# Optimization experiments

Hardware: AMD Instinct MI355X
Metric: run time of the kernel (lower is better)

The kernel has to match this reference:

```python
import jax, jax.numpy as jnp
import numpy as np

EPS_FEAT = 1e-4   # stabilizer eps inside favorp_projection
EPS_DEN = 0.01    # clamp_min eps for the attention denominator


def favorp_projection(data, projection_matrix, is_query):
    # data: [b, h, n, d]; projection_matrix: [h, m, d]
    d = data.shape[-1]
    data_normalizer = d ** (-0.25)
    ratio = projection_matrix.shape[1] ** (-0.5)
    data_dash = jnp.einsum('bhnd,hmd->bhnm', data_normalizer * data, projection_matrix)
    diag_data = (jnp.sum(data * data, axis=-1) * 0.5 * data_normalizer * data_normalizer)[..., None]
    if is_query:
        stabilizer = jax.lax.stop_gradient(jnp.max(data_dash, axis=-1, keepdims=True))
    else:
        stabilizer = jax.lax.stop_gradient(jnp.max(data_dash, axis=(-1, -2), keepdims=True))
    return ratio * jnp.exp(data_dash - diag_data - stabilizer) + EPS_FEAT


def setup_inputs() -> dict:
    key = jax.random.key(0)
    ks = jax.random.split(key, 12)
    N, B, E, H, D, M = 4096, 4, 1024, 16, 64, 64
    s = E ** -0.5
    return {
        'query': jax.random.normal(ks[0], (N, B, E), jnp.float32),
        'key': jax.random.normal(ks[1], (N, B, E), jnp.float32),
        'value': jax.random.normal(ks[2], (N, B, E), jnp.float32),
        'Wq': jax.random.normal(ks[3], (E, E), jnp.float32) * s,
        'bq': jax.random.normal(ks[4], (E,), jnp.float32) * 0.02,
        'Wk': jax.random.normal(ks[5], (E, E), jnp.float32) * s,
        'bk': jax.random.normal(ks[6], (E,), jnp.float32) * 0.02,
        'Wv': jax.random.normal(ks[7], (E, E), jnp.float32) * s,
        'bv': jax.random.normal(ks[8], (E,), jnp.float32) * 0.02,
        'Wo': jax.random.normal(ks[9], (E, E), jnp.float32) * s,
        'bo': jax.random.normal(ks[10], (E,), jnp.float32) * 0.02,
        'proj': jax.random.normal(ks[11], (H, M, D), jnp.float32),
    }


def reference(query, key, value, Wq, bq, Wk, bk, Wv, bv, Wo, bo, proj):
    H = proj.shape[0]
    # [n, b, e] -> [b, n, e]
    q_in = query.transpose(1, 0, 2)
    k_in = key.transpose(1, 0, 2)
    v_in = value.transpose(1, 0, 2)
    B, N, E = q_in.shape
    D = E // H

    def lin(x, W, b):
        return jnp.einsum('bne,fe->bnf', x, W) + b

    def split_heads(x):  # [b, n, e] -> [b, h, n, d]
        return x.reshape(B, N, H, D).transpose(0, 2, 1, 3)

    q = split_heads(lin(q_in, Wq, bq))
    k = split_heads(lin(k_in, Wk, bk))
    v = split_heads(lin(v_in, Wv, bv))

    q_prime = favorp_projection(q, proj, is_query=True)   # [b, h, n, m]
    k_prime = favorp_projection(k, proj, is_query=False)  # [b, h, n, m]

    # non-causal linear attention: O(n * m * d)
    kv = jnp.einsum('bhnm,bhnd->bhmd', k_prime, v)
    qkv = jnp.einsum('bhnm,bhmd->bhnd', q_prime, kv)
    normalizer = jnp.einsum('bhnm,bhm->bhn', q_prime, k_prime.sum(axis=2))
    output = qkv / jnp.maximum(normalizer[..., None], EPS_DEN)

    attn_output = output.transpose(0, 2, 1, 3).reshape(B, N, E)  # b h n d -> b n (h d)
    out = lin(attn_output, Wo, bo)
    return out.transpose(1, 0, 2)  # back to [n, b, e]
```

## Files before the change

kernel.cpp:

```cpp
#include <hip/hip_runtime.h>
#include <math.h>

#define B_   4
#define N_   4096
#define E_   1024
#define H_   16
#define BN_  (B_*N_)
#define BH_  (B_*H_)
#define SPLITK 8

#define NRM_C   0.35355339059327373f
#define DIAG_C  0.0625f
#define RATIO_C 0.125f
#define EPSF    1e-4f
#define EPSD    0.01f

typedef __attribute__((ext_vector_type(8))) short bf16x8;
typedef __attribute__((ext_vector_type(4))) float f32x4;

__device__ __forceinline__ unsigned short f32_to_bf16(float x) {
    unsigned int u = __float_as_uint(x);
    unsigned int r = (u + 0x7fffu + ((u >> 16) & 1u)) >> 16;
    return (unsigned short)r;
}
__device__ __forceinline__ float bf16_to_f32(unsigned short h) {
    return __uint_as_float(((unsigned int)h) << 16);
}

__device__ __forceinline__ void atomicMaxF(float* addr, float v) {
    if (v >= 0.f) atomicMax((int*)addr, __float_as_int(v));
    else          atomicMin((unsigned int*)addr, __float_as_uint(v));
}

__global__ void init_stab(float* stab) {
    if (threadIdx.x < BH_) stab[threadIdx.x] = -INFINITY;
}

template<int IN_MODE>
__global__ __launch_bounds__(256) void convert_split(const float* __restrict__ src,
                                                     unsigned short* __restrict__ hi,
                                                     unsigned short* __restrict__ lo,
                                                     int total4)
{
    int i = blockIdx.x * 256 + threadIdx.x;
    const int stride = gridDim.x * 256;
    for (; i < total4; i += stride) {
        long e4 = (long)i * 4;
        const float* p;
        if (IN_MODE == 0) {
            long r = e4 >> 10; int e = (int)(e4 & 1023);
            int b = (int)(r >> 12), n = (int)(r & 4095);
            p = src + (((long)(n * B_ + b)) << 10) + e;
        } else {
            p = src + e4;
        }
        float4 v = *(const float4*)p;
        ushort4 h, l;
        h.x = f32_to_bf16(v.x); l.x = f32_to_bf16(v.x - bf16_to_f32(h.x));
        h.y = f32_to_bf16(v.y); l.y = f32_to_bf16(v.y - bf16_to_f32(h.y));
        h.z = f32_to_bf16(v.z); l.z = f32_to_bf16(v.z - bf16_to_f32(h.z));
        h.w = f32_to_bf16(v.w); l.w = f32_to_bf16(v.w - bf16_to_f32(h.w));
        *(ushort4*)(hi + e4) = h;
        *(ushort4*)(lo + e4) = l;
    }
}

__device__ __forceinline__ void gl_lds16(const unsigned short* g, unsigned short* l) {
    __builtin_amdgcn_global_load_lds((const __attribute__((address_space(1))) void*)g,
                                     (__attribute__((address_space(3))) void*)l, 16, 0, 0);
}

#define SMEM_BYTES (4*64*68*4 + 2*4*64*4)

template<int MODE>
__global__ __launch_bounds__(256) void gemm_mfma(const unsigned short* __restrict__ Ahi,
                                                 const unsigned short* __restrict__ Alo,
                                                 const unsigned short* __restrict__ Bhi,
                                                 const unsigned short* __restrict__ Blo,
                                                 const float* __restrict__ bias,
                                                 float* __restrict__ Y,
                                                 float* __restrict__ stab,
                                                 const unsigned short* __restrict__ PShi,
                                                 const unsigned short* __restrict__ PSlo,
                                                 const unsigned short* __restrict__ kvThi,
                                                 const unsigned short* __restrict__ kvTlo,
                                                 const float* __restrict__ ksum,
                                                 unsigned short* __restrict__ AttnHi,
                                                 unsigned short* __restrict__ AttnLo)
{
    __shared__ __align__(16) char SMEM[SMEM_BYTES];
    unsigned short* smem = (unsigned short*)SMEM;
    const int t = threadIdx.x;
    const int w = t >> 6, lane = t & 63;
    const int row0 = blockIdx.x * 128, col0 = blockIdx.y * 128;
    const int wrow = (w >> 1) * 64, wcol = (w & 1) * 64;
    const int g = lane >> 4, rl = lane & 15;

    const int sr = w * 32 + (lane >> 2);
    const int kswz = (((lane & 3) ^ ((lane >> 2) & 3)) << 3);
    const long aoff = (long)(row0 + sr) * E_ + kswz;
    const long boff = (long)(col0 + sr) * E_ + kswz;

    f32x4 acc[4][4];
#pragma unroll
    for (int m = 0; m < 4; ++m)
#pragma unroll
        for (int n = 0; n < 4; ++n) acc[m][n] = (f32x4){0.f, 0.f, 0.f, 0.f};

#define STAGE_STEP(KS, BUF)                                                          \
    {                                                                                \
        const int k0 = (KS) * 32;                                                    \
        unsigned short* d = smem + (BUF) * 16384 + w * 1024;                         \
        gl_lds16(Ahi + aoff + k0,             d);                                    \
        gl_lds16(Ahi + aoff + k0 + 16 * E_,   d + 512);                              \
        gl_lds16(Alo + aoff + k0,             d + 4096);                             \
        gl_lds16(Alo + aoff + k0 + 16 * E_,   d + 4096 + 512);                       \
        gl_lds16(Bhi + boff + k0,             d + 8192);                             \
        gl_lds16(Bhi + boff + k0 + 16 * E_,   d + 8192 + 512);                       \
        gl_lds16(Blo + boff + k0,             d + 12288);                            \
        gl_lds16(Blo + boff + k0 + 16 * E_,   d + 12288 + 512);                      \
    }

    STAGE_STEP(0, 0);

    for (int ks = 0; ks < 32; ++ks) {
        __syncthreads();
        if (ks + 1 < 32) STAGE_STEP(ks + 1, (ks + 1) & 1);
        const unsigned short* sb = smem + (ks & 1) * 16384;
        bf16x8 ah[4], al[4], bh[4], bl[4];
#pragma unroll
        for (int m = 0; m < 4; ++m) {
            int r = wrow + m * 16 + rl;
            int off = r * 32 + ((g ^ (r & 3)) << 3);
            ah[m] = *(const bf16x8*)(sb + off);
            al[m] = *(const bf16x8*)(sb + 4096 + off);
        }
#pragma unroll
        for (int n = 0; n < 4; ++n) {
            int r = wcol + n * 16 + rl;
            int off = r * 32 + ((g ^ (r & 3)) << 3);
            bh[n] = *(const bf16x8*)(sb + 8192 + off);
            bl[n] = *(const bf16x8*)(sb + 12288 + off);
        }
#pragma unroll
        for (int m = 0; m < 4; ++m)
#pragma unroll
            for (int n = 0; n < 4; ++n)
                acc[m][n] = __builtin_amdgcn_mfma_f32_16x16x32_bf16(ah[m], bh[n], acc[m][n], 0, 0, 0);
#pragma unroll
        for (int m = 0; m < 4; ++m)
#pragma unroll
            for (int n = 0; n < 4; ++n)
                acc[m][n] = __builtin_amdgcn_mfma_f32_16x16x32_bf16(ah[m], bl[n], acc[m][n], 0, 0, 0);
#pragma unroll
        for (int m = 0; m < 4; ++m)
#pragma unroll
            for (int n = 0; n < 4; ++n)
                acc[m][n] = __builtin_amdgcn_mfma_f32_16x16x32_bf16(al[m], bh[n], acc[m][n], 0, 0, 0);
    }
#undef STAGE_STEP

    float bv[4];
#pragma unroll
    for (int n = 0; n < 4; ++n) bv[n] = bias[col0 + wcol + n * 16 + rl];

    if (MODE <= 1) {
#pragma unroll
        for (int m = 0; m < 4; ++m) {
            int rbase = row0 + wrow + m * 16 + g * 4;
#pragma unroll
            for (int n = 0; n < 4; ++n) {
                int c = col0 + wcol + n * 16 + rl;
#pragma unroll
                for (int q = 0; q < 4; ++q) {
                    int r = rbase + q;
                    float v = acc[m][n][q] + bv[n];
                    long off;
                    if (MODE == 0) off = (long)r * E_ + c;
                    else { int b = r >> 12, nn = r & (N_ - 1); off = (long)(nn * B_ + b) * E_ + c; }
                    Y[off] = v;
                }
            }
        }
        return;
    }

    __syncthreads();
    float* accF  = (float*)SMEM + w * (64 * 68);
    float* diagL = (float*)(SMEM + 4*64*68*4) + w * 64;
    float* rnmL  = (float*)(SMEM + 4*64*68*4) + 256 + w * 64;
    const int b_idx = row0 >> 12;
    const int hg = (col0 >> 6) + (w & 1);
    const int bh = b_idx * H_ + hg;

#pragma unroll
    for (int m = 0; m < 4; ++m)
#pragma unroll
        for (int n = 0; n < 4; ++n)
#pragma unroll
            for (int q = 0; q < 4; ++q)
                accF[(m*16 + g*4 + q) * 68 + n*16 + rl] = acc[m][n][q] + bv[n];
    {
        float s = 0.f;
#pragma unroll 16
        for (int d = 0; d < 64; ++d) { float x = accF[lane * 68 + d]; s = fmaf(x, x, s); }
        diagL[lane] = s * DIAG_C;
    }
    __syncthreads();

    float wavemax = -INFINITY;
#pragma unroll
    for (int mi = 0; mi < 4; ++mi) {
        bf16x8 dah[2], dal[2];
#pragma unroll
        for (int kk = 0; kk < 2; ++kk) {
            const float* src = &accF[(mi*16 + rl) * 68 + kk*32 + g*8];
            float4 f0 = *(const float4*)src, f1 = *(const float4*)(src + 4);
            float fv[8] = {f0.x,f0.y,f0.z,f0.w,f1.x,f1.y,f1.z,f1.w};
            bf16x8 hh, ll;
#pragma unroll
            for (int j = 0; j < 8; ++j) {
                unsigned short h16 = f32_to_bf16(fv[j]);
                hh[j] = (short)h16;
                ll[j] = (short)f32_to_bf16(fv[j] - bf16_to_f32(h16));
            }
            dah[kk] = hh; dal[kk] = ll;
        }
        f32x4 dacc[4];
#pragma unroll
        for (int n = 0; n < 4; ++n) dacc[n] = (f32x4){0.f,0.f,0.f,0.f};
#pragma unroll
        for (int n = 0; n < 4; ++n)
#pragma unroll
            for (int kk = 0; kk < 2; ++kk) {
                long po = (long)hg * 4096 + (n*16 + rl) * 64 + kk*32 + g*8;
                bf16x8 pbh = *(const bf16x8*)(PShi + po);
                bf16x8 pbl = *(const bf16x8*)(PSlo + po);
                dacc[n] = __builtin_amdgcn_mfma_f32_16x16x32_bf16(dah[kk], pbh, dacc[n], 0, 0, 0);
                dacc[n] = __builtin_amdgcn_mfma_f32_16x16x32_bf16(dah[kk], pbl, dacc[n], 0, 0, 0);
                dacc[n] = __builtin_amdgcn_mfma_f32_16x16x32_bf16(dal[kk], pbh, dacc[n], 0, 0, 0);
            }
        if (MODE == 2) {
#pragma unroll
            for (int n = 0; n < 4; ++n)
#pragma unroll
                for (int q = 0; q < 4; ++q) {
                    float dsh = dacc[n][q] * NRM_C;
                    wavemax = fmaxf(wavemax, dsh);
                    int rloc = mi*16 + g*4 + q;
                    Y[(long)(row0 + wrow + rloc) * E_ + col0 + wcol + n*16 + rl] = dsh - diagL[rloc];
                }
        } else {
            float rm0 = -INFINITY, rm1 = -INFINITY, rm2 = -INFINITY, rm3 = -INFINITY;
#pragma unroll
            for (int n = 0; n < 4; ++n) {
                rm0 = fmaxf(rm0, dacc[n][0]); rm1 = fmaxf(rm1, dacc[n][1]);
                rm2 = fmaxf(rm2, dacc[n][2]); rm3 = fmaxf(rm3, dacc[n][3]);
            }
#pragma unroll
            for (int off = 1; off < 16; off <<= 1) {
                rm0 = fmaxf(rm0, __shfl_xor(rm0, off));
                rm1 = fmaxf(rm1, __shfl_xor(rm1, off));
                rm2 = fmaxf(rm2, __shfl_xor(rm2, off));
                rm3 = fmaxf(rm3, __shfl_xor(rm3, off));
            }
            float rmq[4] = {rm0 * NRM_C, rm1 * NRM_C, rm2 * NRM_C, rm3 * NRM_C};
#pragma unroll
            for (int n = 0; n < 4; ++n)
#pragma unroll
                for (int q = 0; q < 4; ++q) {
                    int rloc = mi*16 + g*4 + q;
                    float qp = RATIO_C * expf(dacc[n][q] * NRM_C - diagL[rloc] - rmq[q]) + EPSF;
                    accF[rloc * 68 + n*16 + rl] = qp;
                }
        }
    }

    if (MODE == 2) {
#pragma unroll
        for (int off = 1; off < 64; off <<= 1) wavemax = fmaxf(wavemax, __shfl_xor(wavemax, off));
        if (lane == 0) atomicMaxF(&stab[bh], wavemax);
        return;
    }

    {
        float s = 0.f;
        const float* kb = ksum + bh * 64;
#pragma unroll 16
        for (int m = 0; m < 64; ++m) s = fmaf(accF[lane * 68 + m], kb[m], s);
        rnmL[lane] = 1.f / fmaxf(s, EPSD);
    }
    __syncthreads();
#pragma unroll
    for (int mi = 0; mi < 4; ++mi) {
        bf16x8 qah[2], qal[2];
#pragma unroll
        for (int kk = 0; kk < 2; ++kk) {
            const float* src = &accF[(mi*16 + rl) * 68 + kk*32 + g*8];
            float4 f0 = *(const float4*)src, f1 = *(const float4*)(src + 4);
            float fv[8] = {f0.x,f0.y,f0.z,f0.w,f1.x,f1.y,f1.z,f1.w};
            bf16x8 hh, ll;
#pragma unroll
            for (int j = 0; j < 8; ++j) {
                unsigned short h16 = f32_to_bf16(fv[j]);
                hh[j] = (short)h16;
                ll[j] = (short)f32_to_bf16(fv[j] - bf16_to_f32(h16));
            }
            qah[kk] = hh; qal[kk] = ll;
        }
        f32x4 oacc[4];
#pragma unroll
        for (int n = 0; n < 4; ++n) oacc[n] = (f32x4){0.f,0.f,0.f,0.f};
#pragma unroll
        for (int n = 0; n < 4; ++n)
#pragma unroll
            for (int kk = 0; kk < 2; ++kk) {
                long ko = (long)bh * 4096 + (n*16 + rl) * 64 + kk*32 + g*8;
                bf16x8 kbh = *(const bf16x8*)(kvThi + ko);
                bf16x8 kbl = *(const bf16x8*)(kvTlo + ko);
                oacc[n] = __builtin_amdgcn_mfma_f32_16x16x32_bf16(qah[kk], kbh, oacc[n], 0, 0, 0);
                oacc[n] = __builtin_amdgcn_mfma_f32_16x16x32_bf16(qah[kk], kbl, oacc[n], 0, 0, 0);
                oacc[n] = __builtin_amdgcn_mfma_f32_16x16x32_bf16(qal[kk], kbh, oacc[n], 0, 0, 0);
            }
#pragma unroll
        for (int n = 0; n < 4; ++n)
#pragma unroll
            for (int q = 0; q < 4; ++q) {
                int rloc = mi*16 + g*4 + q;
                float o = oacc[n][q] * rnmL[rloc];
                long off = (long)(row0 + wrow + rloc) * E_ + col0 + wcol + n*16 + rl;
                unsigned short h16 = f32_to_bf16(o);
                AttnHi[off] = h16;
                AttnLo[off] = f32_to_bf16(o - bf16_to_f32(h16));
            }
    }
}

template<int IN_MODE, int OUT_MODE>
__global__ __launch_bounds__(256) void lin_gemm(const float* __restrict__ X,
                                                const float* __restrict__ W,
                                                const float* __restrict__ bias,
                                                float* __restrict__ Y)
{
    __shared__ float As[16][68];
    __shared__ float Ws[16][68];
    const int row0 = blockIdx.x * 64;
    const int col0 = blockIdx.y * 64;
    const int t  = threadIdx.x;
    const int lr = t >> 2;
    const int lk = (t & 3) * 4;
    const int ty = t >> 4, tx = t & 15;

    long arow;
    {
        int r = row0 + lr;
        if (IN_MODE == 0) { int b = r >> 12, n = r & (N_ - 1); arow = (long)(n * B_ + b) * E_; }
        else              { arow = (long)r * E_; }
    }
    const long wrow = (long)(col0 + lr) * E_;

    float acc[4][4] = {};
    for (int e0 = 0; e0 < E_; e0 += 16) {
        float4 av = *(const float4*)(X + arow + e0 + lk);
        float4 wv = *(const float4*)(W + wrow + e0 + lk);
        As[lk+0][lr] = av.x; As[lk+1][lr] = av.y; As[lk+2][lr] = av.z; As[lk+3][lr] = av.w;
        Ws[lk+0][lr] = wv.x; Ws[lk+1][lr] = wv.y; Ws[lk+2][lr] = wv.z; Ws[lk+3][lr] = wv.w;
        __syncthreads();
#pragma unroll
        for (int k = 0; k < 16; ++k) {
            float4 a = *(const float4*)&As[k][ty*4];
            float4 w = *(const float4*)&Ws[k][tx*4];
            float a_[4] = {a.x,a.y,a.z,a.w};
            float w_[4] = {w.x,w.y,w.z,w.w};
#pragma unroll
            for (int i = 0; i < 4; ++i)
#pragma unroll
                for (int j = 0; j < 4; ++j)
                    acc[i][j] = fmaf(a_[i], w_[j], acc[i][j]);
        }
        __syncthreads();
    }
    float4 bvv = *(const float4*)(bias + col0 + tx*4);
    float b_[4] = {bvv.x,bvv.y,bvv.z,bvv.w};
#pragma unroll
    for (int i = 0; i < 4; ++i) {
        int r = row0 + ty*4 + i;
        float4 o;
        o.x = acc[i][0] + b_[0]; o.y = acc[i][1] + b_[1];
        o.z = acc[i][2] + b_[2]; o.w = acc[i][3] + b_[3];
        long off;
        if (OUT_MODE == 0) off = (long)r * E_ + col0 + tx*4;
        else { int b = r >> 12, n = r & (N_ - 1); off = (long)(n * B_ + b) * E_ + col0 + tx*4; }
        *(float4*)(Y + off) = o;
    }
}

template<int IS_QUERY>
__global__ __launch_bounds__(256) void favorp_dash(float* __restrict__ Xh,
                                                   const float* __restrict__ proj,
                                                   float* __restrict__ stab)
{
    __shared__ float Xs[64][68];
    __shared__ float Ps[64][68];
    __shared__ float diag[64];
    __shared__ float red4[4];
    __shared__ float rowred[64][17];
    const int bh = blockIdx.x, b = bh >> 4, h = bh & 15;
    const int n0 = blockIdx.y * 64;
    const int t = threadIdx.x;
    const int r = t >> 2, c0 = (t & 3) * 16;
    const int ty = t >> 4, tx = t & 15;

    const float* xrow = Xh + (long)(b * N_ + n0 + r) * E_ + h * 64;
    const float* prow = proj + (long)(h * 64 + r) * 64;
#pragma unroll
    for (int c = 0; c < 4; ++c) {
        float4 v = *(const float4*)(xrow + c0 + c*4);
        Xs[c0+c*4+0][r] = v.x; Xs[c0+c*4+1][r] = v.y; Xs[c0+c*4+2][r] = v.z; Xs[c0+c*4+3][r] = v.w;
        float4 p = *(const float4*)(prow + c0 + c*4);
        Ps[c0+c*4+0][r] = p.x; Ps[c0+c*4+1][r] = p.y; Ps[c0+c*4+2][r] = p.z; Ps[c0+c*4+3][r] = p.w;
    }
    __syncthreads();
    if (t < 64) {
        float s = 0.f;
#pragma unroll 16
        for (int d = 0; d < 64; ++d) { float x = Xs[d][t]; s = fmaf(x, x, s); }
        diag[t] = s * DIAG_C;
    }
    __syncthreads();

    float acc[4][4] = {};
#pragma unroll 16
    for (int d = 0; d < 64; ++d) {
        float4 a = *(const float4*)&Xs[d][ty*4];
        float4 p = *(const float4*)&Ps[d][tx*4];
        float a_[4] = {a.x,a.y,a.z,a.w};
        float p_[4] = {p.x,p.y,p.z,p.w};
#pragma unroll
        for (int i = 0; i < 4; ++i)
#pragma unroll
            for (int j = 0; j < 4; ++j)
                acc[i][j] = fmaf(a_[i], p_[j], acc[i][j]);
    }
    float dash[4][4];
#pragma unroll
    for (int i = 0; i < 4; ++i)
#pragma unroll
        for (int j = 0; j < 4; ++j) dash[i][j] = acc[i][j] * NRM_C;

    if (IS_QUERY) {
#pragma unroll
        for (int i = 0; i < 4; ++i) {
            float m = fmaxf(fmaxf(dash[i][0], dash[i][1]), fmaxf(dash[i][2], dash[i][3]));
            rowred[ty*4+i][tx] = m;
        }
        __syncthreads();
#pragma unroll
        for (int i = 0; i < 4; ++i) {
            int row = ty*4 + i;
            float m = rowred[row][0];
#pragma unroll
            for (int jj = 1; jj < 16; ++jj) m = fmaxf(m, rowred[row][jj]);
            float dg = diag[row];
            float4 o;
            o.x = RATIO_C * expf(dash[i][0] - dg - m) + EPSF;
            o.y = RATIO_C * expf(dash[i][1] - dg - m) + EPSF;
            o.z = RATIO_C * expf(dash[i][2] - dg - m) + EPSF;
            o.w = RATIO_C * expf(dash[i][3] - dg - m) + EPSF;
            *(float4*)(Xh + (long)(b * N_ + n0 + row) * E_ + h * 64 + tx*4) = o;
        }
    } else {
        float lmax = dash[0][0];
#pragma unroll
        for (int i = 0; i < 4; ++i)
#pragma unroll
            for (int j = 0; j < 4; ++j) lmax = fmaxf(lmax, dash[i][j]);
#pragma unroll
        for (int i = 0; i < 4; ++i) {
            int row = ty*4 + i;
            float dg = diag[row];
            float4 o = { dash[i][0]-dg, dash[i][1]-dg, dash[i][2]-dg, dash[i][3]-dg };
            *(float4*)(Xh + (long)(b * N_ + n0 + row) * E_ + h * 64 + tx*4) = o;
        }
#pragma unroll
        for (int off = 32; off > 0; off >>= 1) lmax = fmaxf(lmax, __shfl_down(lmax, off));
        if ((t & 63) == 0) red4[t >> 6] = lmax;
        __syncthreads();
        if (t == 0)
            atomicMaxF(&stab[bh], fmaxf(fmaxf(red4[0], red4[1]), fmaxf(red4[2], red4[3])));
    }
}

__global__ __launch_bounds__(256) void kv_partial(const float* __restrict__ T1,
                                                  const float* __restrict__ V,
                                                  const float* __restrict__ stab,
                                                  float* __restrict__ kvp,
                                                  float* __restrict__ ksump)
{
    __shared__ float KPs[16][68];
    __shared__ float Vs[16][68];
    const int bh = blockIdx.x, chunk = blockIdx.y;
    const int b = bh >> 4, h = bh & 15;
    const int t = threadIdx.x;
    const int lr = t >> 4, lm = (t & 15) * 4;
    const int ty = t >> 4, tx = t & 15;
    const float stb = stab[bh];
    float acc[4][4] = {};
    float ks = 0.f;
    const int nbeg = chunk * (N_ / SPLITK), nend = nbeg + (N_ / SPLITK);
    for (int n0 = nbeg; n0 < nend; n0 += 16) {
        long rowoff = (long)(b * N_ + n0 + lr) * E_ + h * 64 + lm;
        float4 tv = *(const float4*)(T1 + rowoff);
        float4 vv = *(const float4*)(V + rowoff);
        KPs[lr][lm+0] = RATIO_C * expf(tv.x - stb) + EPSF;
        KPs[lr][lm+1] = RATIO_C * expf(tv.y - stb) + EPSF;
        KPs[lr][lm+2] = RATIO_C * expf(tv.z - stb) + EPSF;
        KPs[lr][lm+3] = RATIO_C * expf(tv.w - stb) + EPSF;
        *(float4*)&Vs[lr][lm] = vv;
        __syncthreads();
        if (t < 64) {
#pragma unroll
            for (int rr = 0; rr < 16; ++rr) ks += KPs[rr][t];
        }
#pragma unroll
        for (int k = 0; k < 16; ++k) {
            float4 a = *(const float4*)&KPs[k][ty*4];
            float4 v4 = *(const float4*)&Vs[k][tx*4];
            float a_[4] = {a.x,a.y,a.z,a.w};
            float v_[4] = {v4.x,v4.y,v4.z,v4.w};
#pragma unroll
            for (int i = 0; i < 4; ++i)
#pragma unroll
                for (int j = 0; j < 4; ++j)
                    acc[i][j] = fmaf(a_[i], v_[j], acc[i][j]);
        }
        __syncthreads();
    }
    const long kvbase = ((long)chunk * BH_ + bh) * 4096;
#pragma unroll
    for (int i = 0; i < 4; ++i) {
        float4 o = {acc[i][0], acc[i][1], acc[i][2], acc[i][3]};
        *(float4*)(kvp + kvbase + (ty*4+i) * 64 + tx*4) = o;
    }
    if (t < 64) ksump[((long)chunk * BH_ + bh) * 64 + t] = ks;
}

__global__ __launch_bounds__(256) void kv_reduce(const float* __restrict__ kvp,
                                                 const float* __restrict__ ksump,
                                                 float* __restrict__ kvM,
                                                 float* __restrict__ ksum,
                                                 unsigned short* __restrict__ kvThi,
                                                 unsigned short* __restrict__ kvTlo)
{
    int idx = blockIdx.x * 256 + threadIdx.x;
    if (idx < BH_ * 4096) {
        float s = 0.f;
#pragma unroll
        for (int c = 0; c < SPLITK; ++c) s += kvp[(long)c * BH_ * 4096 + idx];
        kvM[idx] = s;
        int bh = idx >> 12, md = idx & 4095, m = md >> 6, d = md & 63;
        unsigned short h16 = f32_to_bf16(s);
        long toff = (long)bh * 4096 + d * 64 + m;
        kvThi[toff] = h16;
        kvTlo[toff] = f32_to_bf16(s - bf16_to_f32(h16));
    } else {
        int j = idx - BH_ * 4096;
        if (j < BH_ * 64) {
            float s = 0.f;
#pragma unroll
            for (int c = 0; c < SPLITK; ++c) s += ksump[(long)c * BH_ * 64 + j];
            ksum[j] = s;
        }
    }
}

__global__ __launch_bounds__(256) void qkv_attn(const float* __restrict__ Qp,
                                                const float* __restrict__ kvM,
                                                const float* __restrict__ ksum,
                                                float* __restrict__ attn)
{
    __shared__ float QPs[64][68];
    __shared__ float kvs[64][68];
    __shared__ float ksums[64];
    __shared__ float rnorm[64];
    const int bh = blockIdx.x, b = bh >> 4, h = bh & 15;
    const int n0 = blockIdx.y * 64;
    const int t = threadIdx.x;
    const int r = t >> 2, c0 = (t & 3) * 16;
    const int ty = t >> 4, tx = t & 15;

#pragma unroll
    for (int c = 0; c < 4; ++c) {
        int idx = t * 16 + c * 4;
        float4 v = *(const float4*)(kvM + (long)bh * 4096 + idx);
        *(float4*)&kvs[idx >> 6][idx & 63] = v;
    }
    if (t < 64) ksums[t] = ksum[bh * 64 + t];
    const float* qrow = Qp + (long)(b * N_ + n0 + r) * E_ + h * 64;
#pragma unroll
    for (int c = 0; c < 4; ++c) {
        float4 v = *(const float4*)(qrow + c0 + c*4);
        QPs[c0+c*4+0][r] = v.x; QPs[c0+c*4+1][r] = v.y; QPs[c0+c*4+2][r] = v.z; QPs[c0+c*4+3][r] = v.w;
    }
    __syncthreads();
    if (t < 64) {
        float s = 0.f;
#pragma unroll 16
        for (int m = 0; m < 64; ++m) s = fmaf(QPs[m][t], ksums[m], s);
        rnorm[t] = 1.f / fmaxf(s, EPSD);
    }
    __syncthreads();
    float acc[4][4] = {};
#pragma unroll 16
    for (int m = 0; m < 64; ++m) {
        float4 a = *(const float4*)&QPs[m][ty*4];
        float4 v4 = *(const float4*)&kvs[m][tx*4];
        float a_[4] = {a.x,a.y,a.z,a.w};
        float v_[4] = {v4.x,v4.y,v4.z,v4.w};
#pragma unroll
        for (int i = 0; i < 4; ++i)
#pragma unroll
            for (int j = 0; j < 4; ++j)
                acc[i][j] = fmaf(a_[i], v_[j], acc[i][j]);
    }
#pragma unroll
    for (int i = 0; i < 4; ++i) {
        int row = ty*4 + i;
        float rn = rnorm[row];
        float4 o = {acc[i][0]*rn, acc[i][1]*rn, acc[i][2]*rn, acc[i][3]*rn};
        *(float4*)(attn + (long)(b * N_ + n0 + row) * E_ + h * 64 + tx*4) = o;
    }
}

extern "C" void kernel_launch(void* const* d_in, const int* in_sizes, int n_in,
                              void* d_out, int out_size, void* d_ws, size_t ws_size,
                              hipStream_t stream)
{
    const float* query = (const float*)d_in[0];
    const float* key   = (const float*)d_in[1];
    const float* value = (const float*)d_in[2];
    const float* Wq    = (const float*)d_in[3];
    const float* bq    = (const float*)d_in[4];
    const float* Wk    = (const float*)d_in[5];
    const float* bk    = (const float*)d_in[6];
    const float* Wv    = (const float*)d_in[7];
    const float* bv    = (const float*)d_in[8];
    const float* Wo    = (const float*)d_in[9];
    const float* bo    = (const float*)d_in[10];
    const float* proj  = (const float*)d_in[11];
    float* O = (float*)d_out;

    float* ws = (float*)d_ws;
    const size_t SZ = (size_t)BN_ * E_;
    float* A     = ws;
    float* kvp   = ws + SZ;
    float* ksump = kvp + (size_t)SPLITK * BH_ * 4096;
    float* kvM   = ksump + (size_t)SPLITK * BH_ * 64;
    float* ksum  = kvM + (size_t)BH_ * 4096;
    float* stab  = ksum + (size_t)BH_ * 64;
    unsigned short* kvThi = (unsigned short*)(stab + 64);
    unsigned short* kvTlo = kvThi + (size_t)BH_ * 4096;
    unsigned short* PShi  = kvTlo + (size_t)BH_ * 4096;
    unsigned short* PSlo  = PShi + 65536;
    const size_t COMMON = SZ + (size_t)SPLITK * BH_ * 4096 + (size_t)SPLITK * BH_ * 64
                        + (size_t)BH_ * 4096 + (size_t)BH_ * 64 + 64
                        + ((size_t)BH_ * 4096)  + 65536 / 2 * 2 / 2 * 0 + 32768 * 2 / 2;
    const size_t EXTRA_F = (size_t)BH_ * 4096  + 65536 ;
    const size_t COMMON_F = SZ + (size_t)SPLITK * BH_ * 4096 + (size_t)SPLITK * BH_ * 64
                          + (size_t)BH_ * 4096 + (size_t)BH_ * 64 + 64 + EXTRA_F;
    unsigned short* Xhi = (unsigned short*)(ws + COMMON_F);
    unsigned short* Xlo = Xhi + SZ;
    unsigned short* Whi = Xlo + SZ;
    unsigned short* Wlo = Whi + (size_t)E_ * E_;
    const size_t NEED_FAST = (COMMON_F + SZ + (size_t)E_ * E_) * 4;
    (void)COMMON;

    dim3 gF(BH_, N_ / 64);
    dim3 gKV(BH_, SPLITK);
    const int nRed = (BH_ * 4096 + BH_ * 64) / 256;

    if (ws_size >= NEED_FAST) {
        dim3 gG(BN_ / 128, E_ / 128);
        const int X4 = (int)(SZ / 4), W4 = (E_ * E_) / 4;
        unsigned short* AttnHi = (unsigned short*)A;
        unsigned short* AttnLo = AttnHi + SZ;

        convert_split<1><<<64, 256, 0, stream>>>(proj, PShi, PSlo, 16384);
        init_stab<<<1, 64, 0, stream>>>(stab);
        convert_split<0><<<2048, 256, 0, stream>>>(key, Xhi, Xlo, X4);
        convert_split<1><<<1024, 256, 0, stream>>>(Wk, Whi, Wlo, W4);
        gemm_mfma<2><<<gG, 256, 0, stream>>>(Xhi, Xlo, Whi, Wlo, bk, O, stab,
                                             PShi, PSlo, nullptr, nullptr, nullptr, nullptr, nullptr);
        convert_split<0><<<2048, 256, 0, stream>>>(value, Xhi, Xlo, X4);
        convert_split<1><<<1024, 256, 0, stream>>>(Wv, Whi, Wlo, W4);
        gemm_mfma<0><<<gG, 256, 0, stream>>>(Xhi, Xlo, Whi, Wlo, bv, A, nullptr,
                                             nullptr, nullptr, nullptr, nullptr, nullptr, nullptr, nullptr);
        kv_partial<<<gKV, 256, 0, stream>>>(O, A, stab, kvp, ksump);
        kv_reduce<<<nRed, 256, 0, stream>>>(kvp, ksump, kvM, ksum, kvThi, kvTlo);
        convert_split<0><<<2048, 256, 0, stream>>>(query, Xhi, Xlo, X4);
        convert_split<1><<<1024, 256, 0, stream>>>(Wq, Whi, Wlo, W4);
        gemm_mfma<3><<<gG, 256, 0, stream>>>(Xhi, Xlo, Whi, Wlo, bq, nullptr, nullptr,
                                             PShi, PSlo, kvThi, kvTlo, ksum, AttnHi, AttnLo);
        convert_split<1><<<1024, 256, 0, stream>>>(Wo, Whi, Wlo, W4);
        gemm_mfma<1><<<gG, 256, 0, stream>>>(AttnHi, AttnLo, Whi, Wlo, bo, O, nullptr,
                                             nullptr, nullptr, nullptr, nullptr, nullptr, nullptr, nullptr);
    } else {
        dim3 gGemm(BN_ / 64, E_ / 64);
        lin_gemm<0,0><<<gGemm, 256, 0, stream>>>(key, Wk, bk, O);
        init_stab<<<1, 64, 0, stream>>>(stab);
        favorp_dash<0><<<gF, 256, 0, stream>>>(O, proj, stab);
        lin_gemm<0,0><<<gGemm, 256, 0, stream>>>(value, Wv, bv, A);
        kv_partial<<<gKV, 256, 0, stream>>>(O, A, stab, kvp, ksump);
        kv_reduce<<<nRed, 256, 0, stream>>>(kvp, ksump, kvM, ksum, kvThi, kvTlo);
        lin_gemm<0,0><<<gGemm, 256, 0, stream>>>(query, Wq, bq, O);
        favorp_dash<1><<<gF, 256, 0, stream>>>(O, proj, stab);
        qkv_attn<<<gF, 256, 0, stream>>>(O, kvM, ksum, A);
        lin_gemm<1,1><<<gGemm, 256, 0, stream>>>(A, Wo, bo, O);
    }
}
```

Before: 625.3 us.

## Fuse fp32 input split-to-bf16 into GEMM A-tile loads, drop convert passes

The three input projections now stream fp32 activations straight into LDS, reading through the [n,b,e] layout with an XOR swizzle. Each A fragment is split into hi/lo bf16 in registers using packed v_cvt_pk_bf16_f32 instructions. This removes three separate convert_split passes over the 64MB inputs and their hi/lo intermediate buffers. In exchange the A tile in LDS is fp32, so each thread reads twice as many bytes per k-step and does the split ALU work inside the main loop. The epilogue splits also switch to the packed-conversion helper.

Result: slower. 666.6 us (+6.6%).

```diff
diff --git a/kernel.cpp b/kernel.cpp
--- a/kernel.cpp
+++ b/kernel.cpp
@@ -25,6 +25,27 @@
 }
 __device__ __forceinline__ float bf16_to_f32(unsigned short h) {
     return __uint_as_float(((unsigned int)h) << 16);
+}
+
+__device__ __forceinline__ unsigned int pk_bf16(float a, float b) {
+    unsigned int r;
+    asm("v_cvt_pk_bf16_f32 %0, %1, %2" : "=v"(r) : "v"(a), "v"(b));
+    return r;
+}
+
+__device__ __forceinline__ void f32x8_split(float4 fa, float4 fb, bf16x8& hi, bf16x8& lo) {
+    unsigned int h0 = pk_bf16(fa.x, fa.y), h1 = pk_bf16(fa.z, fa.w);
+    unsigned int h2 = pk_bf16(fb.x, fb.y), h3 = pk_bf16(fb.z, fb.w);
+    float e0 = __uint_as_float(h0 << 16), e1 = __uint_as_float(h0 & 0xffff0000u);
+    float e2 = __uint_as_float(h1 << 16), e3 = __uint_as_float(h1 & 0xffff0000u);
+    float e4 = __uint_as_float(h2 << 16), e5 = __uint_as_float(h2 & 0xffff0000u);
+    float e6 = __uint_as_float(h3 << 16), e7 = __uint_as_float(h3 & 0xffff0000u);
+    unsigned int l0 = pk_bf16(fa.x - e0, fa.y - e1), l1 = pk_bf16(fa.z - e2, fa.w - e3);
+    unsigned int l2 = pk_bf16(fb.x - e4, fb.y - e5), l3 = pk_bf16(fb.z - e6, fb.w - e7);
+    union { unsigned int u[4]; bf16x8 v; } H, L;
+    H.u[0] = h0; H.u[1] = h1; H.u[2] = h2; H.u[3] = h3;
+    L.u[0] = l0; L.u[1] = l1; L.u[2] = l2; L.u[3] = l3;
+    hi = H.v; lo = L.v;
 }
 
 __device__ __forceinline__ void atomicMaxF(float* addr, float v) {
@@ -65,18 +86,19 @@
     }
 }
 
-__device__ __forceinline__ void gl_lds16(const unsigned short* g, unsigned short* l) {
+__device__ __forceinline__ void gl_lds16(const void* g, void* l) {
     __builtin_amdgcn_global_load_lds((const __attribute__((address_space(1))) void*)g,
                                      (__attribute__((address_space(3))) void*)l, 16, 0, 0);
 }
 
 #define SMEM_BYTES (4*64*68*4 + 2*4*64*4)
 
-template<int MODE>
+template<int MODE, int ASRC>
 __global__ __launch_bounds__(256) void gemm_mfma(const unsigned short* __restrict__ Ahi,
                                                  const unsigned short* __restrict__ Alo,
                                                  const unsigned short* __restrict__ Bhi,
                                                  const unsigned short* __restrict__ Blo,
+                                                 const float* __restrict__ Afp,
                                                  const float* __restrict__ bias,
                                                  float* __restrict__ Y,
                                                  float* __restrict__ stab,
@@ -98,8 +120,23 @@
 
     const int sr = w * 32 + (lane >> 2);
     const int kswz = (((lane & 3) ^ ((lane >> 2) & 3)) << 3);
-    const long aoff = (long)(row0 + sr) * E_ + kswz;
     const long boff = (long)(col0 + sr) * E_ + kswz;
+
+    long aoff = 0;
+    long aS[4]; int aD[4];
+    if (ASRC == 0) {
+        aoff = (long)(row0 + sr) * E_ + kswz;
+    } else {
+#pragma unroll
+        for (int i = 0; i < 4; ++i) {
+            int slot = i * 256 + t;
+            int r = slot >> 3, gl = slot & 7;
+            int rg = row0 + r;
+            int nn = rg & (N_ - 1), bb = rg >> 12;
+            aS[i] = (long)(nn * B_ + bb) * E_ + ((gl ^ (r & 7)) << 2);
+            aD[i] = (i * 256 + w * 64) << 3;
+        }
+    }
 
     f32x4 acc[4][4];
 #pragma unroll
@@ -109,16 +146,24 @@
 
 #define STAGE_STEP(KS, BUF)                                                          \
     {                                                                                \
-        const int k0 = (KS) * 32;                                                    \
-        unsigned short* d = smem + (BUF) * 16384 + w * 1024;                         \
-        gl_lds16(Ahi + aoff + k0,             d);                                    \
-        gl_lds16(Ahi + aoff + k0 + 16 * E_,   d + 512);                              \
-        gl_lds16(Alo + aoff + k0,             d + 4096);                             \
-        gl_lds16(Alo + aoff + k0 + 16 * E_,   d + 4096 + 512);                       \
-        gl_lds16(Bhi + boff + k0,             d + 8192);                             \
-        gl_lds16(Bhi + boff + k0 + 16 * E_,   d + 8192 + 512);                       \
-        gl_lds16(Blo + boff + k0,             d + 12288);                            \
-        gl_lds16(Blo + boff + k0 + 16 * E_,   d + 12288 + 512);                      \
+        const int k0_ = (KS) * 32;                                                   \
+        unsigned short* bu_ = smem + (BUF) * 16384;                                  \
+        if (ASRC == 1) {                                                             \
+            _Pragma("unroll")                                                        \
+            for (int i_ = 0; i_ < 4; ++i_)                                           \
+                gl_lds16(Afp + aS[i_] + k0_, bu_ + aD[i_]);                          \
+        } else {                                                                     \
+            unsigned short* d_ = bu_ + w * 1024;                                     \
+            gl_lds16(Ahi + aoff + k0_,           d_);                                \
+            gl_lds16(Ahi + aoff + k0_ + 16*E_,   d_ + 512);                          \
+            gl_lds16(Alo + aoff + k0_,           d_ + 4096);                         \
+            gl_lds16(Alo + aoff + k0_ + 16*E_,   d_ + 4096 + 512);                   \
+        }                                                                            \
+        unsigned short* db_ = bu_ + w * 1024;                                        \
+        gl_lds16(Bhi + boff + k0_,           db_ + 8192);                            \
+        gl_lds16(Bhi + boff + k0_ + 16*E_,   db_ + 8192 + 512);                      \
+        gl_lds16(Blo + boff + k0_,           db_ + 12288);                           \
+        gl_lds16(Blo + boff + k0_ + 16*E_,   db_ + 12288 + 512);                     \
     }
 
     STAGE_STEP(0, 0);
@@ -128,19 +173,31 @@
         if (ks + 1 < 32) STAGE_STEP(ks + 1, (ks + 1) & 1);
         const unsigned short* sb = smem + (ks & 1) * 16384;
         bf16x8 ah[4], al[4], bh[4], bl[4];
-#pragma unroll
-        for (int m = 0; m < 4; ++m) {
-            int r = wrow + m * 16 + rl;
-            int off = r * 32 + ((g ^ (r & 3)) << 3);
-            ah[m] = *(const bf16x8*)(sb + off);
-            al[m] = *(const bf16x8*)(sb + 4096 + off);
+        if (ASRC == 1) {
+#pragma unroll
+            for (int m = 0; m < 4; ++m) {
+                int r_ = wrow + m * 16 + rl;
+                int x7 = r_ & 7;
+                const unsigned short* rowp = sb + r_ * 64;
+                float4 fa = *(const float4*)(rowp + (((2*g + 0) ^ x7) << 3));
+                float4 fb = *(const float4*)(rowp + (((2*g + 1) ^ x7) << 3));
+                f32x8_split(fa, fb, ah[m], al[m]);
+            }
+        } else {
+#pragma unroll
+            for (int m = 0; m < 4; ++m) {
+                int r_ = wrow + m * 16 + rl;
+                int off_ = r_ * 32 + ((g ^ (r_ & 3)) << 3);
+                ah[m] = *(const bf16x8*)(sb + off_);
+                al[m] = *(const bf16x8*)(sb + 4096 + off_);
+            }
         }
 #pragma unroll
         for (int n = 0; n < 4; ++n) {
-            int r = wcol + n * 16 + rl;
-            int off = r * 32 + ((g ^ (r & 3)) << 3);
-            bh[n] = *(const bf16x8*)(sb + 8192 + off);
-            bl[n] = *(const bf16x8*)(sb + 12288 + off);
+            int r_ = wcol + n * 16 + rl;
+            int off_ = r_ * 32 + ((g ^ (r_ & 3)) << 3);
+            bh[n] = *(const bf16x8*)(sb + 8192 + off_);
+            bl[n] = *(const bf16x8*)(sb + 12288 + off_);
         }
 #pragma unroll
         for (int m = 0; m < 4; ++m)
@@ -191,7 +248,7 @@
     float* rnmL  = (float*)(SMEM + 4*64*68*4) + 256 + w * 64;
     const int b_idx = row0 >> 12;
     const int hg = (col0 >> 6) + (w & 1);
-    const int bh = b_idx * H_ + hg;
+    const int bh_i = b_idx * H_ + hg;
 
 #pragma unroll
     for (int m = 0; m < 4; ++m)
@@ -216,15 +273,7 @@
         for (int kk = 0; kk < 2; ++kk) {
             const float* src = &accF[(mi*16 + rl) * 68 + kk*32 + g*8];
             float4 f0 = *(const float4*)src, f1 = *(const float4*)(src + 4);
-            float fv[8] = {f0.x,f0.y,f0.z,f0.w,f1.x,f1.y,f1.z,f1.w};
-            bf16x8 hh, ll;
-#pragma unroll
-            for (int j = 0; j < 8; ++j) {
-                unsigned short h16 = f32_to_bf16(fv[j]);
-                hh[j] = (short)h16;
-                ll[j] = (short)f32_to_bf16(fv[j] - bf16_to_f32(h16));
-            }
-            dah[kk] = hh; dal[kk] = ll;
+            f32x8_split(f0, f1, dah[kk], dal[kk]);
         }
         f32x4 dacc[4];
 #pragma unroll
@@ -279,13 +328,13 @@
     if (MODE == 2) {
 #pragma unroll
         for (int off = 1; off < 64; off <<= 1) wavemax = fmaxf(wavemax, __shfl_xor(wavemax, off));
-        if (lane == 0) atomicMaxF(&stab[bh], wavemax);
+        if (lane == 0) atomicMaxF(&stab[bh_i], wavemax);
         return;
     }
 
     {
         float s = 0.f;
-        const float* kb = ksum + bh * 64;
+        const float* kb = ksum + bh_i * 64;
 #pragma unroll 16
         for (int m = 0; m < 64; ++m) s = fmaf(accF[lane * 68 + m], kb[m], s);
         rnmL[lane] = 1.f / fmaxf(s, EPSD);
@@ -298,15 +347,7 @@
         for (int kk = 0; kk < 2; ++kk) {
             const float* src = &accF[(mi*16 + rl) * 68 + kk*32 + g*8];
             float4 f0 = *(const float4*)src, f1 = *(const float4*)(src + 4);
-            float fv[8] = {f0.x,f0.y,f0.z,f0.w,f1.x,f1.y,f1.z,f1.w};
-            bf16x8 hh, ll;
-#pragma unroll
-            for (int j = 0; j < 8; ++j) {
-                unsigned short h16 = f32_to_bf16(fv[j]);
-                hh[j] = (short)h16;
-                ll[j] = (short)f32_to_bf16(fv[j] - bf16_to_f32(h16));
-            }
-            qah[kk] = hh; qal[kk] = ll;
+            f32x8_split(f0, f1, qah[kk], qal[kk]);
         }
         f32x4 oacc[4];
 #pragma unroll
@@ -315,7 +356,7 @@
         for (int n = 0; n < 4; ++n)
 #pragma unroll
             for (int kk = 0; kk < 2; ++kk) {
-                long ko = (long)bh * 4096 + (n*16 + rl) * 64 + kk*32 + g*8;
+                long ko = (long)bh_i * 4096 + (n*16 + rl) * 64 + kk*32 + g*8;
                 bf16x8 kbh = *(const bf16x8*)(kvThi + ko);
                 bf16x8 kbl = *(const bf16x8*)(kvTlo + ko);
                 oacc[n] = __builtin_amdgcn_mfma_f32_16x16x32_bf16(qah[kk], kbh, oacc[n], 0, 0, 0);
@@ -662,18 +703,12 @@
     unsigned short* kvTlo = kvThi + (size_t)BH_ * 4096;
     unsigned short* PShi  = kvTlo + (size_t)BH_ * 4096;
     unsigned short* PSlo  = PShi + 65536;
-    const size_t COMMON = SZ + (size_t)SPLITK * BH_ * 4096 + (size_t)SPLITK * BH_ * 64
-                        + (size_t)BH_ * 4096 + (size_t)BH_ * 64 + 64
-                        + ((size_t)BH_ * 4096)  + 65536 / 2 * 2 / 2 * 0 + 32768 * 2 / 2;
     const size_t EXTRA_F = (size_t)BH_ * 4096  + 65536 ;
     const size_t COMMON_F = SZ + (size_t)SPLITK * BH_ * 4096 + (size_t)SPLITK * BH_ * 64
                           + (size_t)BH_ * 4096 + (size_t)BH_ * 64 + 64 + EXTRA_F;
-    unsigned short* Xhi = (unsigned short*)(ws + COMMON_F);
-    unsigned short* Xlo = Xhi + SZ;
-    unsigned short* Whi = Xlo + SZ;
+    unsigned short* Whi = (unsigned short*)(ws + COMMON_F);
     unsigned short* Wlo = Whi + (size_t)E_ * E_;
-    const size_t NEED_FAST = (COMMON_F + SZ + (size_t)E_ * E_) * 4;
-    (void)COMMON;
+    const size_t NEED_FAST = (COMMON_F + (size_t)E_ * E_) * 4;
 
     dim3 gF(BH_, N_ / 64);
     dim3 gKV(BH_, SPLITK);
@@ -681,29 +716,26 @@
 
     if (ws_size >= NEED_FAST) {
         dim3 gG(BN_ / 128, E_ / 128);
-        const int X4 = (int)(SZ / 4), W4 = (E_ * E_) / 4;
+        const int W4 = (E_ * E_) / 4;
         unsigned short* AttnHi = (unsigned short*)A;
         unsigned short* AttnLo = AttnHi + SZ;
 
         convert_split<1><<<64, 256, 0, stream>>>(proj, PShi, PSlo, 16384);
         init_stab<<<1, 64, 0, stream>>>(stab);
-        convert_split<0><<<2048, 256, 0, stream>>>(key, Xhi, Xlo, X4);
         convert_split<1><<<1024, 256, 0, stream>>>(Wk, Whi, Wlo, W4);
-        gemm_mfma<2><<<gG, 256, 0, stream>>>(Xhi, Xlo, Whi, Wlo, bk, O, stab,
-                                             PShi, PSlo, nullptr, nullptr, nullptr, nullptr, nullptr);
-        convert_split<0><<<2048, 256, 0, stream>>>(value, Xhi, Xlo, X4);
+        gemm_mfma<2,1><<<gG, 256, 0, stream>>>(nullptr, nullptr, Whi, Wlo, key, bk, O, stab,
+                                               PShi, PSlo, nullptr, nullptr, nullptr, nullptr, nullptr);
         convert_split<1><<<1024, 256, 0, stream>>>(Wv, Whi, Wlo, W4);
-        gemm_mfma<0><<<gG, 256, 0, stream>>>(Xhi, Xlo, Whi, Wlo, bv, A, nullptr,
-                                             nullptr, nullptr, nullptr, nullptr, nullptr, nullptr, nullptr);
+        gemm_mfma<0,1><<<gG, 256, 0, stream>>>(nullptr, nullptr, Whi, Wlo, value, bv, A, nullptr,
+                                               nullptr, nullptr, nullptr, nullptr, nullptr, nullptr, nullptr);
         kv_partial<<<gKV, 256, 0, stream>>>(O, A, stab, kvp, ksump);
         kv_reduce<<<nRed, 256, 0, stream>>>(kvp, ksump, kvM, ksum, kvThi, kvTlo);
-        convert_split<0><<<2048, 256, 0, stream>>>(query, Xhi, Xlo, X4);
         convert_split<1><<<1024, 256, 0, stream>>>(Wq, Whi, Wlo, W4);
-        gemm_mfma<3><<<gG, 256, 0, stream>>>(Xhi, Xlo, Whi, Wlo, bq, nullptr, nullptr,
-                                             PShi, PSlo, kvThi, kvTlo, ksum, AttnHi, AttnLo);
+        gemm_mfma<3,1><<<gG, 256, 0, stream>>>(nullptr, nullptr, Whi, Wlo, query, bq, nullptr, nullptr,
+                                               PShi, PSlo, kvThi, kvTlo, ksum, AttnHi, AttnLo);
         convert_split<1><<<1024, 256, 0, stream>>>(Wo, Whi, Wlo, W4);
-        gemm_mfma<1><<<gG, 256, 0, stream>>>(AttnHi, AttnLo, Whi, Wlo, bo, O, nullptr,
-                                             nullptr, nullptr, nullptr, nullptr, nullptr, nullptr, nullptr);
+        gemm_mfma<1,0><<<gG, 256, 0, stream>>>(AttnHi, AttnLo, Whi, Wlo, nullptr, bo, O, nullptr,
+                                               nullptr, nullptr, nullptr, nullptr, nullptr, nullptr, nullptr);
     } else {
         dim3 gGemm(BN_ / 64, E_ / 64);
         lin_gemm<0,0><<<gGemm, 256, 0, stream>>>(key, Wk, bk, O);
```
